# Optimization experiments

Hardware: AMD Instinct MI355X
Metric: run time of the kernel (lower is better)

Reference implementation:

```python
import jax, jax.numpy as jnp
import numpy as np
from jax import lax

K = 5          # dynamic kernel size
GROUPS = 8     # inter_channels // group_channels = 128 // 16
R = 2          # pixel shuffle upscale factor
SLOPE = 0.01   # LeakyReLU default negative_slope
EPS = 1e-5     # BatchNorm eps


def conv2d(x, w, b, pad=0):
    # x: [B,C,H,W], w: [O,I,kh,kw]
    y = lax.conv_general_dilated(x, w, (1, 1), [(pad, pad), (pad, pad)],
                                 dimension_numbers=('NCHW', 'OIHW', 'NCHW'))
    return y + b[None, :, None, None]


def pixel_shuffle(x, r):
    B, C, H, W = x.shape
    x = x.reshape(B, C // (r * r), r, r, H, W)
    x = x.transpose(0, 1, 4, 2, 5, 3)  # B, C', H, r, W, r
    return x.reshape(B, C // (r * r), H * r, W * r)


def involution(x, weight, k, groups, pad):
    # x: [B,C,H,W]; weight: [B,groups,k,k,H,W]
    # out[b, g*gc+c, h, w] = sum_ij weight[b,g,i,j,h,w] * x_pad[b, g*gc+c, h+i, w+j]
    B, C, H, W = x.shape
    gc = C // groups
    xp = jnp.pad(x, ((0, 0), (0, 0), (pad, pad), (pad, pad)))
    xg = xp.reshape(B, groups, gc, H + 2 * pad, W + 2 * pad)
    out = jnp.zeros((B, groups, gc, H, W), x.dtype)
    for i in range(k):
        for j in range(k):
            out = out + weight[:, :, None, i, j] * xg[:, :, :, i:i + H, j:j + W]
    return out.reshape(B, C, H, W)


def setup_inputs() -> dict:
    key = jax.random.key(0)
    ks = jax.random.split(key, 16)
    s = 0.05
    return {
        'high_level': jax.random.normal(ks[0], (8, 128, 64, 64), jnp.float32),
        'low_level': jax.random.normal(ks[1], (8, 224, 128, 128), jnp.float32),
        'emb': jax.random.normal(ks[2], (8, 256, 128, 128), jnp.float32),
        'reduce_w': jax.random.normal(ks[3], (128, 256, 1, 1), jnp.float32) * s,
        'reduce_b': jax.random.normal(ks[4], (128,), jnp.float32) * s,
        'conv1_w': jax.random.normal(ks[5], (32, 128, 1, 1), jnp.float32) * s,
        'conv1_b': jax.random.normal(ks[6], (32,), jnp.float32) * s,
        'conv2_w': jax.random.normal(ks[7], (200, 32, 3, 3), jnp.float32) * s,
        'conv2_b': jax.random.normal(ks[8], (200,), jnp.float32) * s,
        'embconv_w': jax.random.normal(ks[9], (32, 256, 1, 1), jnp.float32) * s,
        'embconv_b': jax.random.normal(ks[10], (32,), jnp.float32) * s,
        'out_w': jax.random.normal(ks[11], (64, 128, 1, 1), jnp.float32) * s,
        'out_b': jax.random.normal(ks[12], (64,), jnp.float32) * s,
        'bn_gamma': jnp.ones((64,), jnp.float32),
        'bn_beta': jnp.zeros((64,), jnp.float32),
        'bn_mean': jnp.zeros((64,), jnp.float32),
        'bn_var': jax.random.uniform(ks[13], (64,), jnp.float32, 0.5, 1.5),
    }


def reference(high_level, low_level, emb,
              reduce_w, reduce_b, conv1_w, conv1_b, conv2_w, conv2_b,
              embconv_w, embconv_b, out_w, out_b,
              bn_gamma, bn_beta, bn_mean, bn_var):
    cat = jnp.concatenate([pixel_shuffle(high_level, R), low_level], axis=1)
    cat = conv2d(cat, reduce_w, reduce_b)
    mix = jax.nn.leaky_relu(conv2d(cat, conv1_w, conv1_b)
                            + conv2d(emb, embconv_w, embconv_b), SLOPE)
    w = conv2d(mix, conv2_w, conv2_b, pad=1)  # [B, K*K*GROUPS, H, W]
    B, _, H, W = w.shape
    w = w.reshape(B, GROUPS, K, K, H, W)
    o = involution(cat, w, K, GROUPS, (K - 1) // 2)
    o = conv2d(o, out_w, out_b)
    o = (o - bn_mean[None, :, None, None]) * (bn_gamma[None, :, None, None]
        / jnp.sqrt(bn_var[None, :, None, None] + EPS)) + bn_beta[None, :, None, None]
    return jax.nn.leaky_relu(o, SLOPE)
```

## Files before the change

### kernel.cpp

```cpp
#include <hip/hip_runtime.h>

typedef unsigned short u16; typedef unsigned int u32; typedef unsigned long long u64;
typedef __attribute__((ext_vector_type(8))) short short8;
typedef __attribute__((ext_vector_type(16))) float f32x16;

#define HW 16384

#define RED_B  0
#define C1E_B  128
#define C2_B   160
#define OUT_B  416
#define BN_SC  480
#define BN_SH  544
#define FLAG_OFF   4096
#define RWB_OFF    8192
#define C1B_OFF    73728
#define EMBB_OFF   81920
#define OUTB_OFF   98304
#define C2PB_OFF   114688
#define CAT2_OFF   524288
#define MIX_OFF    34078720

__device__ __forceinline__ float bf2f(u16 x){ u32 u=((u32)x)<<16; float f; __builtin_memcpy(&f,&u,4); return f; }
__device__ __forceinline__ u16 f2bf(float f){ u32 u; __builtin_memcpy(&u,&f,4); return (u16)((u + 0x7fffu + ((u>>16)&1u))>>16); }
__device__ __forceinline__ u32 pk2(float a, float b){ return (u32)f2bf(a) | ((u32)f2bf(b)<<16); }
__device__ __forceinline__ float lrelu(float x){ return x>0.f ? x : 0.01f*x; }

template<int M> __device__ __forceinline__ u16 ldb(const void* p, size_t i){
    if (M==1) return ((const u16*)p)[i];
    return f2bf(((const float*)p)[i]);
}
template<int M> __device__ __forceinline__ float ldf(const void* p, size_t i){
    if (M==1) return bf2f(((const u16*)p)[i]);
    return ((const float*)p)[i];
}
__device__ __forceinline__ int swz(int p){ return ((p>>1) ^ (p>>3)) & 7; }

template<int M>
__device__ __forceinline__ void load8x8(const void* p, size_t base, size_t stride, u32 R[8][4]){
    if (M==1){
#pragma unroll
        for (int j=0;j<8;j++)
            __builtin_memcpy(&R[j][0], (const u16*)p + base + (size_t)j*stride, 16);
    } else {
        float raw[8][8];
#pragma unroll
        for (int j=0;j<8;j++)
            __builtin_memcpy(&raw[j][0], (const float*)p + base + (size_t)j*stride, 32);
#pragma unroll
        for (int j=0;j<8;j++)
#pragma unroll
        for (int m=0;m<4;m++) R[j][m] = pk2(raw[j][2*m], raw[j][2*m+1]);
    }
}

__global__ void detect_kernel(const void* __restrict__ emb, u32* __restrict__ flag){
    int tid = threadIdx.x;
    const u16* p = (const u16*)emb;
    int e = (p[tid*2] >> 7) & 0xFF;
    u64 m = __ballot(e >= 100 && e <= 140);
    if (tid == 0) *flag = (__popcll(m) >= 32) ? 1u : 0u;
}

template<int M>
__device__ __forceinline__ void prep_body(
    const void* rw, const void* rb, const void* c1w, const void* c1b,
    const void* c2w, const void* c2b, const void* ew, const void* eb,
    const void* ow, const void* ob, const void* gam, const void* bet,
    const void* mn, const void* vr, char* ws)
{
    float* wf = (float*)ws;
    int i = blockIdx.x*256 + threadIdx.x;
    if (i < 32768) {
        int o = i>>8, ic = i&255;
        int s = ic>>4, qq = (ic>>3)&1, e = ic&7;
        int dst = (((o>>5)*16 + s)*64 + qq*32 + (o&31))*8 + e;
        ((u16*)(ws+RWB_OFF))[dst] = ldb<M>(rw, i);
    }
    else if (i < 36864)  ((u16*)(ws+C1B_OFF))[i-32768] = ldb<M>(c1w, i-32768);
    else if (i < 45056)  ((u16*)(ws+EMBB_OFF))[i-36864] = ldb<M>(ew, i-36864);
    else if (i < 53248)  ((u16*)(ws+OUTB_OFF))[i-45056] = ldb<M>(ow, i-45056);
    else if (i < 126976) {
        int j = i-53248; int o = j/288, k = j - o*288;
        int tap = k>>5, ic = k&31;
        u16 v = 0;
        if (o < 200) v = ldb<M>(c2w, (size_t)o*288 + ic*9 + tap);
        ((u16*)(ws+C2PB_OFF))[j] = v;
    }
    else if (i < 127584) {
        int j = i-126976;
        if (j < 128) wf[RED_B+j] = ldf<M>(rb, j);
        else if (j < 160) wf[C1E_B+j-128] = ldf<M>(c1b, j-128) + ldf<M>(eb, j-128);
        else if (j < 416) { int o = j-160; wf[C2_B+o] = (o<200) ? ldf<M>(c2b,o) : 0.f; }
        else if (j < 480) wf[OUT_B+j-416] = ldf<M>(ob, j-416);
        else if (j < 544) { int c=j-480; wf[BN_SC+c] = ldf<M>(gam,c) * rsqrtf(ldf<M>(vr,c)+1e-5f); }
        else { int c=j-544; wf[BN_SH+c] = ldf<M>(bet,c) - ldf<M>(mn,c)*ldf<M>(gam,c)*rsqrtf(ldf<M>(vr,c)+1e-5f); }
    }
}

__global__ __launch_bounds__(256) void k_prep(
    const void* rw, const void* rb, const void* c1w, const void* c1b,
    const void* c2w, const void* c2b, const void* ew, const void* eb,
    const void* ow, const void* ob, const void* gam, const void* bet,
    const void* mn, const void* vr, char* ws, const u32* __restrict__ flag)
{
    if (*flag) prep_body<1>(rw,rb,c1w,c1b,c2w,c2b,ew,eb,ow,ob,gam,bet,mn,vr,ws);
    else       prep_body<0>(rw,rb,c1w,c1b,c2w,c2b,ew,eb,ow,ob,gam,bet,mn,vr,ws);
}

template<int M>
__device__ __forceinline__ void rm_body(
    const void* __restrict__ hi, const void* __restrict__ lo, const void* __restrict__ emb,
    const u16* __restrict__ rwB, const u16* __restrict__ c1B, const u16* __restrict__ embB,
    const float* __restrict__ wf, u16* __restrict__ cat2, u16* __restrict__ mixt,
    u16* At, u16* c2l)
{
    const int tid = threadIdx.x, wvi = tid>>6, lane = tid&63;
    const int col = lane&31, q = lane>>5;
    const int gpx = blockIdx.x*64;
    const int b = gpx>>14, p0 = gpx&16383;
    const int h = p0>>7, w0 = p0&127;
    const int co = tid>>3, po = tid&7;

    {
        u32 W[8][4];
        if (co < 28) {
            u32 R[8][4];
            load8x8<M>(lo, ((size_t)(b*224 + 8*co))*HW + p0 + 8*po, HW, R);
#pragma unroll
            for (int p=0;p<8;p++){
                const int u = p>>1, hf = p&1;
#pragma unroll
                for (int m=0;m<4;m++){
                    u32 A0 = R[2*m][u], A1 = R[2*m+1][u];
                    W[p][m] = hf ? ((A0>>16) | (A1 & 0xffff0000u))
                                 : ((A0 & 0xffffu) | (A1<<16));
                }
            }
            const int ch = co + 4;
#pragma unroll
            for (int p=0;p<8;p++){
                int pg = 8*po + p;
                __builtin_memcpy(At + pg*264 + ((ch ^ swz(pg))<<3), &W[p][0], 16);
            }
        } else {
            const int cc0 = (co-28)*8, h2 = (h&1)*2;
            u32 E[8][2], O[8][2];
            if (M==1){
#pragma unroll
                for (int j=0;j<8;j++){
                    int hc = (cc0+j)*4 + h2;
                    size_t src = ((size_t)(b*128 + hc))*4096 + (size_t)(h>>1)*64 + (w0>>1) + 4*po;
                    __builtin_memcpy(&E[j][0], (const u16*)hi + src, 8);
                    __builtin_memcpy(&O[j][0], (const u16*)hi + src + 4096, 8);
                }
            } else {
                float rE[8][4], rO[8][4];
#pragma unroll
                for (int j=0;j<8;j++){
                    int hc = (cc0+j)*4 + h2;
                    size_t src = ((size_t)(b*128 + hc))*4096 + (size_t)(h>>1)*64 + (w0>>1) + 4*po;
                    __builtin_memcpy(&rE[j][0], (const float*)hi + src, 16);
                    __builtin_memcpy(&rO[j][0], (const float*)hi + src + 4096, 16);
                }
#pragma unroll
                for (int j=0;j<8;j++){
                    E[j][0] = pk2(rE[j][0], rE[j][1]); E[j][1] = pk2(rE[j][2], rE[j][3]);
                    O[j][0] = pk2(rO[j][0], rO[j][1]); O[j][1] = pk2(rO[j][2], rO[j][3]);
                }
            }
#pragma unroll
            for (int p=0;p<8;p++){
                const int k = p>>1, u = k>>1, hf = k&1;
#pragma unroll
                for (int m=0;m<4;m++){
                    u32 A0, A1;
                    if (p&1){ A0 = O[2*m][u]; A1 = O[2*m+1][u]; }
                    else    { A0 = E[2*m][u]; A1 = E[2*m+1][u]; }
                    W[p][m] = hf ? ((A0>>16) | (A1 & 0xffff0000u))
                                 : ((A0 & 0xffffu) | (A1<<16));
                }
            }
            const int ch = co - 28;
#pragma unroll
            for (int p=0;p<8;p++){
                int pg = 8*po + p;
                __builtin_memcpy(At + pg*264 + ((ch ^ swz(pg))<<3), &W[p][0], 16);
            }
        }
    }
    __syncthreads();

    {
        const int rt = (wvi>>1)*32, nc0 = (wvi&1)*64;
        const int pp = rt + col, sw = swz(pp);
        const u16* arow = At + pp*264;
        const int ot0 = (wvi&1)*2;

        f32x16 acc0, acc1;
#pragma unroll
        for (int r=0;r<16;r++){ acc0[r]=0.f; acc1[r]=0.f; }

        short8 Bb[2][8];
#pragma unroll
        for (int nt=0;nt<2;nt++)
#pragma unroll
        for (int s=0;s<8;s++)
            __builtin_memcpy(&Bb[nt][s], rwB + (((size_t)((ot0+nt)*16 + s))*64 + lane)*8, 16);
#pragma unroll
        for (int s=0;s<8;s++){
            short8 a; __builtin_memcpy(&a, arow + (((2*s+q)^sw)<<3), 16);
            acc0 = __builtin_amdgcn_mfma_f32_32x32x16_bf16(a, Bb[0][s], acc0, 0,0,0);
            acc1 = __builtin_amdgcn_mfma_f32_32x32x16_bf16(a, Bb[1][s], acc1, 0,0,0);
        }
#pragma unroll
        for (int nt=0;nt<2;nt++)
#pragma unroll
        for (int s=0;s<8;s++)
            __builtin_memcpy(&Bb[nt][s], rwB + (((size_t)((ot0+nt)*16 + 8+s))*64 + lane)*8, 16);
#pragma unroll
        for (int s=8;s<16;s++){
            short8 a; __builtin_memcpy(&a, arow + (((2*s+q)^sw)<<3), 16);
            acc0 = __builtin_amdgcn_mfma_f32_32x32x16_bf16(a, Bb[0][s-8], acc0, 0,0,0);
            acc1 = __builtin_amdgcn_mfma_f32_32x32x16_bf16(a, Bb[1][s-8], acc1, 0,0,0);
        }

#pragma unroll
        for (int nt=0; nt<2; nt++){
            int oc = nc0 + nt*32 + col;
            float bias = wf[RED_B + oc];
#pragma unroll
            for (int r=0;r<16;r++){
                int row = (r&3) + 8*(r>>2) + 4*q;
                int px = rt + row;
                u16 bv = f2bf((nt ? acc1[r] : acc0[r]) + bias);
                cat2[((size_t)(gpx + px))*128 + oc] = bv;
                c2l[px*136 + (((oc>>3) ^ swz(px))<<3) + (oc&7)] = bv;
            }
        }
    }

    {
        u32 R[8][4];
        load8x8<M>(emb, ((size_t)(b*256 + 8*co))*HW + p0 + 8*po, HW, R);
        u32 W[8][4];
#pragma unroll
        for (int p=0;p<8;p++){
            const int u = p>>1, hf = p&1;
#pragma unroll
            for (int m=0;m<4;m++){
                u32 A0 = R[2*m][u], A1 = R[2*m+1][u];
                W[p][m] = hf ? ((A0>>16) | (A1 & 0xffff0000u))
                             : ((A0 & 0xffffu) | (A1<<16));
            }
        }
        __syncthreads();
#pragma unroll
        for (int p=0;p<8;p++){
            int pg = 8*po + p;
            __builtin_memcpy(At + pg*264 + ((co ^ swz(pg))<<3), &W[p][0], 16);
        }
    }
    __syncthreads();

    const int rt2 = wvi>>1, q2 = wvi&1;
    const int pp2 = rt2*32 + col, sw2 = swz(pp2);
    const u16* arow136 = c2l + pp2*136;
    const u16* arow264 = At + pp2*264;

    f32x16 macc;
#pragma unroll
    for (int r=0;r<16;r++) macc[r]=0.f;

    if (q2 == 0){
        short8 Bc[8];
#pragma unroll
        for (int s=0;s<8;s++)
            __builtin_memcpy(&Bc[s], c1B + (size_t)col*128 + s*16 + q*8, 16);
#pragma unroll
        for (int s=0;s<8;s++){
            short8 a; __builtin_memcpy(&a, arow136 + (((2*s+q)^sw2)<<3), 16);
            macc = __builtin_amdgcn_mfma_f32_32x32x16_bf16(a, Bc[s], macc, 0,0,0);
        }
        short8 Be[4];
#pragma unroll
        for (int s=0;s<4;s++)
            __builtin_memcpy(&Be[s], embB + (size_t)col*256 + s*16 + q*8, 16);
#pragma unroll
        for (int s=0;s<4;s++){
            short8 a; __builtin_memcpy(&a, arow264 + (((2*s+q)^sw2)<<3), 16);
            macc = __builtin_amdgcn_mfma_f32_32x32x16_bf16(a, Be[s], macc, 0,0,0);
        }
    } else {
        short8 Be[12];
#pragma unroll
        for (int s=0;s<12;s++)
            __builtin_memcpy(&Be[s], embB + (size_t)col*256 + (4+s)*16 + q*8, 16);
#pragma unroll
        for (int s=0;s<12;s++){
            int ks = 4 + s;
            short8 a; __builtin_memcpy(&a, arow264 + (((2*ks+q)^sw2)<<3), 16);
            macc = __builtin_amdgcn_mfma_f32_32x32x16_bf16(a, Be[s], macc, 0,0,0);
        }
    }
    __syncthreads();

    float* exch = (float*)At;
    if (q2 == 1){
#pragma unroll
        for (int r=0;r<16;r++){
            int row = (r&3) + 8*(r>>2) + 4*q;
            exch[rt2*1024 + row*32 + col] = macc[r];
        }
    }
    __syncthreads();
    if (q2 == 0){
        float bias = wf[C1E_B + col];
#pragma unroll
        for (int r=0;r<16;r++){
            int row = (r&3) + 8*(r>>2) + 4*q;
            float v = macc[r] + exch[rt2*1024 + row*32 + col] + bias;
            mixt[((size_t)(gpx + rt2*32 + row))*32 + col] = f2bf(lrelu(v));
        }
    }
}

__global__ __launch_bounds__(256,2) void k_rm(
    const void* __restrict__ hi, const void* __restrict__ lo, const void* __restrict__ emb,
    const u16* __restrict__ rwB, const u16* __restrict__ c1B, const u16* __restrict__ embB,
    const float* __restrict__ wf, u16* __restrict__ cat2, u16* __restrict__ mixt,
    const u32* __restrict__ flag)
{
    __shared__ u16 At[64*264];
    __shared__ u16 c2l[64*136];
    if (*flag) rm_body<1>(hi, lo, emb, rwB, c1B, embB, wf, cat2, mixt, At, c2l);
    else       rm_body<0>(hi, lo, emb, rwB, c1B, embB, wf, cat2, mixt, At, c2l);
}

template<int M>
__device__ __forceinline__ void inv_body(
    const u16* __restrict__ cat2, const u16* __restrict__ mixt,
    const u16* __restrict__ c2B, const u16* __restrict__ outB,
    const float* __restrict__ wf, void* __restrict__ out,
    u16* halo_m, u16* wgt_l, u16* halo_c, u16* og)
{
    const int tid = threadIdx.x, wvi = tid>>6, lane = tid&63;
    const int col = lane&31, q = lane>>5;
    const int b = blockIdx.y, ty = blockIdx.x>>3, tx = blockIdx.x&7;
    const int py = tid>>4, px = tid&15;

    f32x16 acc[2][2];
#pragma unroll
    for (int i=0;i<2;i++)
#pragma unroll
    for (int j=0;j<2;j++)
#pragma unroll
    for (int r=0;r<16;r++) acc[i][j][r] = 0.f;

#pragma unroll
    for (int i=0;i<6;i++){
        int idx = tid + i*256;
        if (idx < 1296){
            int point = idx>>2, cq = idx&3;
            int y = ty*16 + point/18 - 1, x = tx*16 + point%18 - 1;
            short8 v;
            if (y>=0 && y<128 && x>=0 && x<128)
                __builtin_memcpy(&v, mixt + ((size_t)(b*HW + y*128 + x))*32 + cq*8, 16);
            else { short z=0; v = (short8){z,z,z,z,z,z,z,z}; }
            *(short8*)(halo_m + point*40 + cq*8) = v;
        }
    }
    __syncthreads();

#pragma unroll 1
    for (int g=0; g<8; g++){
        __syncthreads();

        const int o = g*25 + col;
        short8 Bf[18];
#pragma unroll
        for (int s=0;s<18;s++)
            __builtin_memcpy(&Bf[s], c2B + (size_t)o*288 + s*16 + q*8, 16);

#pragma unroll
        for (int i=0;i<4;i++){
            int idx = tid + i*256;
            if (idx < 800){
                int point = idx>>1, cq = idx&1;
                int y = ty*16 + point/20 - 2, x = tx*16 + point%20 - 2;
                short8 v;
                if (y>=0 && y<128 && x>=0 && x<128)
                    __builtin_memcpy(&v, cat2 + ((size_t)(b*HW + y*128 + x))*128 + g*16 + cq*8, 16);
                else { short z=0; v = (short8){z,z,z,z,z,z,z,z}; }
                *(short8*)(halo_c + point*16 + cq*8) = v;
            }
        }

        f32x16 c0, c1;
#pragma unroll
        for (int r=0;r<16;r++){ c0[r]=0.f; c1[r]=0.f; }
        const int p0 = wvi*64 + col, p1 = p0 + 32;
        const int pya = p0>>4, pxa = p0&15, pyb = p1>>4, pxb = p1&15;
#pragma unroll
        for (int s=0;s<18;s++){
            int tap = s>>1, ih = s&1;
            int dy = tap/3, dx = tap%3;
            short8 a0, a1;
            __builtin_memcpy(&a0, halo_m + ((pya+dy)*18 + pxa+dx)*40 + ih*16 + q*8, 16);
            __builtin_memcpy(&a1, halo_m + ((pyb+dy)*18 + pxb+dx)*40 + ih*16 + q*8, 16);
            c0 = __builtin_amdgcn_mfma_f32_32x32x16_bf16(a0, Bf[s], c0, 0,0,0);
            c1 = __builtin_amdgcn_mfma_f32_32x32x16_bf16(a1, Bf[s], c1, 0,0,0);
        }
        {
            float bias = wf[C2_B + o];
#pragma unroll
            for (int rt2=0; rt2<2; rt2++){
                int mb = wvi*64 + rt2*32;
#pragma unroll
                for (int r=0;r<16;r+=2){
                    int row0 = (r&3) + 8*(r>>2) + 4*q;
                    float v0 = (rt2 ? c1[r]   : c0[r])   + bias;
                    float v1 = (rt2 ? c1[r+1] : c0[r+1]) + bias;
                    u32 pkv = (u32)f2bf(v0) | ((u32)f2bf(v1)<<16);
                    *(u32*)(wgt_l + (size_t)col*264 + mb + row0) = pkv;
                }
            }
        }
        __syncthreads();

        float wvv[25];
#pragma unroll
        for (int t=0;t<25;t++) wvv[t] = bf2f(wgt_l[t*264 + tid]);

        float a16[16];
#pragma unroll
        for (int cc=0;cc<16;cc++) a16[cc]=0.f;
#pragma unroll
        for (int t=0;t<25;t++){
            int dy = t/5, dx = t%5;
            u32 vv[8];
            __builtin_memcpy(vv, halo_c + ((py+dy)*20 + px+dx)*16, 32);
            float wt = wvv[t];
#pragma unroll
            for (int r=0;r<8;r++){
                u32 u = vv[r];
                u32 ulo = u<<16, uhi = u & 0xffff0000u;
                float x0, x1;
                __builtin_memcpy(&x0,&ulo,4); __builtin_memcpy(&x1,&uhi,4);
                a16[2*r]   += wt*x0;
                a16[2*r+1] += wt*x1;
            }
        }
        u32 pk[8];
#pragma unroll
        for (int r=0;r<8;r++) pk[r] = (u32)f2bf(a16[2*r]) | ((u32)f2bf(a16[2*r+1])<<16);
        __builtin_memcpy(og + tid*16, pk, 32);
        __syncthreads();

        short8 bo0, bo1;
        __builtin_memcpy(&bo0, outB + (size_t)(col)*128      + g*16 + q*8, 16);
        __builtin_memcpy(&bo1, outB + (size_t)(32+col)*128   + g*16 + q*8, 16);
#pragma unroll
        for (int rt2=0; rt2<2; rt2++){
            int prow = (wvi*2 + rt2)*32 + col;
            short8 a; __builtin_memcpy(&a, og + prow*16 + q*8, 16);
            acc[rt2][0] = __builtin_amdgcn_mfma_f32_32x32x16_bf16(a, bo0, acc[rt2][0], 0,0,0);
            acc[rt2][1] = __builtin_amdgcn_mfma_f32_32x32x16_bf16(a, bo1, acc[rt2][1], 0,0,0);
        }
    }
#pragma unroll
    for (int rt2=0; rt2<2; rt2++)
#pragma unroll
    for (int nt=0; nt<2; nt++){
        int oc = nt*32 + col;
        float bias = wf[OUT_B+oc], sc = wf[BN_SC+oc], sh = wf[BN_SH+oc];
#pragma unroll
        for (int r=0;r<16;r++){
            int row = (r&3) + 8*(r>>2) + 4*q;
            int p = (wvi*2 + rt2)*32 + row;
            int yy = ty*16 + (p>>4), xx = tx*16 + (p&15);
            float v = lrelu((acc[rt2][nt][r] + bias)*sc + sh);
            size_t oidx = ((size_t)(b*64 + oc))*HW + yy*128 + xx;
            if (M==1) ((u16*)out)[oidx] = f2bf(v);
            else ((float*)out)[oidx] = v;
        }
    }
}

__global__ __launch_bounds__(256,2) void k_inv(
    const u16* __restrict__ cat2, const u16* __restrict__ mixt,
    const u16* __restrict__ c2B, const u16* __restrict__ outB,
    const float* __restrict__ wf, void* __restrict__ out, const u32* __restrict__ flag)
{
    __shared__ u16 halo_m[324*40];
    __shared__ u16 wgt_l[32*264];
    __shared__ u16 halo_c[400*16];
    __shared__ u16 og[256*16];
    if (*flag) inv_body<1>(cat2, mixt, c2B, outB, wf, out, halo_m, wgt_l, halo_c, og);
    else       inv_body<0>(cat2, mixt, c2B, outB, wf, out, halo_m, wgt_l, halo_c, og);
}

extern "C" void kernel_launch(void* const* d_in, const int* in_sizes, int n_in,
                              void* d_out, int out_size, void* d_ws, size_t ws_size,
                              hipStream_t stream) {
    const void* hi  = d_in[0];
    const void* lo  = d_in[1];
    const void* emb = d_in[2];
    char* ws = (char*)d_ws;
    float* wf = (float*)ws;
    u32* flag = (u32*)(ws + FLAG_OFF);
    u16* cat2 = (u16*)(ws + CAT2_OFF);
    u16* mixt = (u16*)(ws + MIX_OFF);

    detect_kernel<<<1, 64, 0, stream>>>(emb, flag);

    k_prep<<<499,256,0,stream>>>(d_in[3],d_in[4],d_in[5],d_in[6],d_in[7],d_in[8],
        d_in[9],d_in[10],d_in[11],d_in[12],d_in[13],d_in[14],d_in[15],d_in[16], ws, flag);

    k_rm<<<2048,256,0,stream>>>(hi, lo, emb, (const u16*)(ws+RWB_OFF),
                                (const u16*)(ws+C1B_OFF), (const u16*)(ws+EMBB_OFF),
                                wf, cat2, mixt, flag);

    k_inv<<<dim3(64,8),256,0,stream>>>(cat2, mixt, (const u16*)(ws+C2PB_OFF),
                                       (const u16*)(ws+OUTB_OFF), wf, d_out, flag);
}
```

Before: 396.2 us.

## Fold conv1 into reduce weights and split reduce/mix GEMMs across 512 threads

Precomputes a combined conv1·reduce weight (and folded bias) in the prep kernel, so the mix branch multiplies the raw concatenated input directly instead of waiting for the reduced cat tensor. This removes the dependency and the extra LDS staging buffer. k_rm now runs 512 threads, with half preloading emb while the other half builds the cat tile, and the K dimension split across four waves with a cross-wave reduction. The k_rm kernel is templated on the input-format flag and launched twice, with early exit in the non-matching variant. The folded weight is rounded to bf16, which changes numerics slightly.

```diff
diff --git a/kernel.cpp b/kernel.cpp
--- a/kernel.cpp
+++ b/kernel.cpp
@@ -18,6 +18,7 @@
 #define EMBB_OFF   81920
 #define OUTB_OFF   98304
 #define C2PB_OFF   114688
+#define WEFF_OFF   262144
 #define CAT2_OFF   524288
 #define MIX_OFF    34078720
 
@@ -35,24 +36,6 @@
     return ((const float*)p)[i];
 }
 __device__ __forceinline__ int swz(int p){ return ((p>>1) ^ (p>>3)) & 7; }
-
-template<int M>
-__device__ __forceinline__ void load8x8(const void* p, size_t base, size_t stride, u32 R[8][4]){
-    if (M==1){
-#pragma unroll
-        for (int j=0;j<8;j++)
-            __builtin_memcpy(&R[j][0], (const u16*)p + base + (size_t)j*stride, 16);
-    } else {
-        float raw[8][8];
-#pragma unroll
-        for (int j=0;j<8;j++)
-            __builtin_memcpy(&raw[j][0], (const float*)p + base + (size_t)j*stride, 32);
-#pragma unroll
-        for (int j=0;j<8;j++)
-#pragma unroll
-        for (int m=0;m<4;m++) R[j][m] = pk2(raw[j][2*m], raw[j][2*m+1]);
-    }
-}
 
 __global__ void detect_kernel(const void* __restrict__ emb, u32* __restrict__ flag){
     int tid = threadIdx.x;
@@ -90,11 +73,26 @@
     else if (i < 127584) {
         int j = i-126976;
         if (j < 128) wf[RED_B+j] = ldf<M>(rb, j);
-        else if (j < 160) wf[C1E_B+j-128] = ldf<M>(c1b, j-128) + ldf<M>(eb, j-128);
+        else if (j < 160) {
+            int o = j-128;
+            float s = ldf<M>(c1b,o) + ldf<M>(eb,o);
+#pragma unroll 8
+            for (int ic=0; ic<128; ic++)
+                s += ldf<M>(c1w, (size_t)o*128+ic) * ldf<M>(rb, ic);
+            wf[C1E_B+o] = s;
+        }
         else if (j < 416) { int o = j-160; wf[C2_B+o] = (o<200) ? ldf<M>(c2b,o) : 0.f; }
         else if (j < 480) wf[OUT_B+j-416] = ldf<M>(ob, j-416);
         else if (j < 544) { int c=j-480; wf[BN_SC+c] = ldf<M>(gam,c) * rsqrtf(ldf<M>(vr,c)+1e-5f); }
         else { int c=j-544; wf[BN_SH+c] = ldf<M>(bet,c) - ldf<M>(mn,c)*ldf<M>(gam,c)*rsqrtf(ldf<M>(vr,c)+1e-5f); }
+    }
+    else if (i < 135776) {
+        int j = i - 127584; int oc = j>>8, k2 = j&255;
+        float s = 0.f;
+#pragma unroll 8
+        for (int ic=0; ic<128; ic++)
+            s += ldf<M>(c1w, (size_t)oc*128+ic) * ldf<M>(rw, (size_t)ic*256+k2);
+        ((u16*)(ws+WEFF_OFF))[oc*256+k2] = f2bf(s);
     }
 }
 
@@ -111,22 +109,68 @@
 template<int M>
 __device__ __forceinline__ void rm_body(
     const void* __restrict__ hi, const void* __restrict__ lo, const void* __restrict__ emb,
-    const u16* __restrict__ rwB, const u16* __restrict__ c1B, const u16* __restrict__ embB,
+    const u16* __restrict__ rwB, const u16* __restrict__ weffB, const u16* __restrict__ embB,
     const float* __restrict__ wf, u16* __restrict__ cat2, u16* __restrict__ mixt,
-    u16* At, u16* c2l)
+    u16* At)
 {
     const int tid = threadIdx.x, wvi = tid>>6, lane = tid&63;
     const int col = lane&31, q = lane>>5;
     const int gpx = blockIdx.x*64;
     const int b = gpx>>14, p0 = gpx&16383;
     const int h = p0>>7, w0 = p0&127;
-    const int co = tid>>3, po = tid&7;
-
-    {
+
+    const int sthr = tid & 255;
+    const int co = sthr>>3, po = sthr&7;
+    const bool is_emb = tid >= 256;
+
+    u32 Wreg[8][4];
+
+    if (is_emb) {
+        u32 R[8][4];
+        size_t base = ((size_t)(b*256 + 8*co))*HW + p0 + 8*po;
+        if (M==1){
+#pragma unroll
+            for (int j=0;j<8;j++)
+                __builtin_memcpy(&R[j][0], (const u16*)emb + base + (size_t)j*HW, 16);
+        } else {
+            float raw[8][8];
+#pragma unroll
+            for (int j=0;j<8;j++)
+                __builtin_memcpy(&raw[j][0], (const float*)emb + base + (size_t)j*HW, 32);
+#pragma unroll
+            for (int j=0;j<8;j++)
+#pragma unroll
+            for (int m=0;m<4;m++) R[j][m] = pk2(raw[j][2*m], raw[j][2*m+1]);
+        }
+#pragma unroll
+        for (int p=0;p<8;p++){
+            const int u = p>>1, hf = p&1;
+#pragma unroll
+            for (int m=0;m<4;m++){
+                u32 A0 = R[2*m][u], A1 = R[2*m+1][u];
+                Wreg[p][m] = hf ? ((A0>>16) | (A1 & 0xffff0000u))
+                                : ((A0 & 0xffffu) | (A1<<16));
+            }
+        }
+    } else {
         u32 W[8][4];
         if (co < 28) {
             u32 R[8][4];
-            load8x8<M>(lo, ((size_t)(b*224 + 8*co))*HW + p0 + 8*po, HW, R);
+            size_t base = ((size_t)(b*224 + 8*co))*HW + p0 + 8*po;
+            if (M==1){
+#pragma unroll
+                for (int j=0;j<8;j++)
+                    __builtin_memcpy(&R[j][0], (const u16*)lo + base + (size_t)j*HW, 16);
+            } else {
+                float raw[8][8];
+#pragma unroll
+                for (int j=0;j<8;j++)
+                    __builtin_memcpy(&raw[j][0], (const float*)lo + base + (size_t)j*HW, 32);
+#pragma unroll
+                for (int j=0;j<8;j++)
+#pragma unroll
+                for (int m=0;m<4;m++) R[j][m] = pk2(raw[j][2*m], raw[j][2*m+1]);
+            }
 #pragma unroll
             for (int p=0;p<8;p++){
                 const int u = p>>1, hf = p&1;
@@ -191,150 +235,100 @@
     }
     __syncthreads();
 
+    const int pt = wvi>>2, ks = wvi&3;
+    const int pp = pt*32 + col, sw = swz(pp);
+    const u16* arow = At + pp*264;
+
+    f32x16 racc, macc;
+#pragma unroll
+    for (int r=0;r<16;r++){ racc[r]=0.f; macc[r]=0.f; }
+
+    short8 Wf[4];
+#pragma unroll
+    for (int t4=0;t4<4;t4++)
+        __builtin_memcpy(&Wf[t4], weffB + (size_t)col*256 + (4*ks+t4)*16 + q*8, 16);
+
+#pragma unroll
+    for (int bt=0; bt<4; bt++){
+        short8 Bb[4];
+#pragma unroll
+        for (int si=0;si<4;si++)
+            __builtin_memcpy(&Bb[si], rwB + (((size_t)(ks*16 + bt*4 + si))*64 + lane)*8, 16);
+#pragma unroll
+        for (int si=0;si<4;si++){
+            int s = bt*4 + si;
+            short8 a; __builtin_memcpy(&a, arow + (((2*s+q)^sw)<<3), 16);
+            racc = __builtin_amdgcn_mfma_f32_32x32x16_bf16(a, Bb[si], racc, 0,0,0);
+            int d = s - 4*ks;
+            if (d>=0 && d<4)
+                macc = __builtin_amdgcn_mfma_f32_32x32x16_bf16(a, Wf[d], macc, 0,0,0);
+        }
+    }
     {
-        const int rt = (wvi>>1)*32, nc0 = (wvi&1)*64;
-        const int pp = rt + col, sw = swz(pp);
-        const u16* arow = At + pp*264;
-        const int ot0 = (wvi&1)*2;
-
-        f32x16 acc0, acc1;
-#pragma unroll
-        for (int r=0;r<16;r++){ acc0[r]=0.f; acc1[r]=0.f; }
-
-        short8 Bb[2][8];
-#pragma unroll
-        for (int nt=0;nt<2;nt++)
-#pragma unroll
-        for (int s=0;s<8;s++)
-            __builtin_memcpy(&Bb[nt][s], rwB + (((size_t)((ot0+nt)*16 + s))*64 + lane)*8, 16);
-#pragma unroll
-        for (int s=0;s<8;s++){
-            short8 a; __builtin_memcpy(&a, arow + (((2*s+q)^sw)<<3), 16);
-            acc0 = __builtin_amdgcn_mfma_f32_32x32x16_bf16(a, Bb[0][s], acc0, 0,0,0);
-            acc1 = __builtin_amdgcn_mfma_f32_32x32x16_bf16(a, Bb[1][s], acc1, 0,0,0);
-        }
-#pragma unroll
-        for (int nt=0;nt<2;nt++)
-#pragma unroll
-        for (int s=0;s<8;s++)
-            __builtin_memcpy(&Bb[nt][s], rwB + (((size_t)((ot0+nt)*16 + 8+s))*64 + lane)*8, 16);
-#pragma unroll
-        for (int s=8;s<16;s++){
-            short8 a; __builtin_memcpy(&a, arow + (((2*s+q)^sw)<<3), 16);
-            acc0 = __builtin_amdgcn_mfma_f32_32x32x16_bf16(a, Bb[0][s-8], acc0, 0,0,0);
-            acc1 = __builtin_amdgcn_mfma_f32_32x32x16_bf16(a, Bb[1][s-8], acc1, 0,0,0);
-        }
-
-#pragma unroll
-        for (int nt=0; nt<2; nt++){
-            int oc = nc0 + nt*32 + col;
-            float bias = wf[RED_B + oc];
-#pragma unroll
-            for (int r=0;r<16;r++){
-                int row = (r&3) + 8*(r>>2) + 4*q;
-                int px = rt + row;
-                u16 bv = f2bf((nt ? acc1[r] : acc0[r]) + bias);
-                cat2[((size_t)(gpx + px))*128 + oc] = bv;
-                c2l[px*136 + (((oc>>3) ^ swz(px))<<3) + (oc&7)] = bv;
-            }
-        }
-    }
-
-    {
-        u32 R[8][4];
-        load8x8<M>(emb, ((size_t)(b*256 + 8*co))*HW + p0 + 8*po, HW, R);
-        u32 W[8][4];
-#pragma unroll
-        for (int p=0;p<8;p++){
-            const int u = p>>1, hf = p&1;
-#pragma unroll
-            for (int m=0;m<4;m++){
-                u32 A0 = R[2*m][u], A1 = R[2*m+1][u];
-                W[p][m] = hf ? ((A0>>16) | (A1 & 0xffff0000u))
-                             : ((A0 & 0xffffu) | (A1<<16));
-            }
-        }
-        __syncthreads();
+        int oc = ks*32 + col;
+        float bias = wf[RED_B + oc];
+#pragma unroll
+        for (int r=0;r<16;r++){
+            int row = (r&3) + 8*(r>>2) + 4*q;
+            cat2[((size_t)(gpx + pt*32 + row))*128 + oc] = f2bf(racc[r] + bias);
+        }
+    }
+    __syncthreads();
+
+    if (is_emb){
 #pragma unroll
         for (int p=0;p<8;p++){
             int pg = 8*po + p;
-            __builtin_memcpy(At + pg*264 + ((co ^ swz(pg))<<3), &W[p][0], 16);
+            __builtin_memcpy(At + pg*264 + ((co ^ swz(pg))<<3), &Wreg[p][0], 16);
         }
     }
     __syncthreads();
 
-    const int rt2 = wvi>>1, q2 = wvi&1;
-    const int pp2 = rt2*32 + col, sw2 = swz(pp2);
-    const u16* arow136 = c2l + pp2*136;
-    const u16* arow264 = At + pp2*264;
-
-    f32x16 macc;
-#pragma unroll
-    for (int r=0;r<16;r++) macc[r]=0.f;
-
-    if (q2 == 0){
-        short8 Bc[8];
-#pragma unroll
-        for (int s=0;s<8;s++)
-            __builtin_memcpy(&Bc[s], c1B + (size_t)col*128 + s*16 + q*8, 16);
-#pragma unroll
-        for (int s=0;s<8;s++){
-            short8 a; __builtin_memcpy(&a, arow136 + (((2*s+q)^sw2)<<3), 16);
-            macc = __builtin_amdgcn_mfma_f32_32x32x16_bf16(a, Bc[s], macc, 0,0,0);
-        }
+    {
         short8 Be[4];
 #pragma unroll
-        for (int s=0;s<4;s++)
-            __builtin_memcpy(&Be[s], embB + (size_t)col*256 + s*16 + q*8, 16);
-#pragma unroll
-        for (int s=0;s<4;s++){
-            short8 a; __builtin_memcpy(&a, arow264 + (((2*s+q)^sw2)<<3), 16);
-            macc = __builtin_amdgcn_mfma_f32_32x32x16_bf16(a, Be[s], macc, 0,0,0);
-        }
-    } else {
-        short8 Be[12];
-#pragma unroll
-        for (int s=0;s<12;s++)
-            __builtin_memcpy(&Be[s], embB + (size_t)col*256 + (4+s)*16 + q*8, 16);
-#pragma unroll
-        for (int s=0;s<12;s++){
-            int ks = 4 + s;
-            short8 a; __builtin_memcpy(&a, arow264 + (((2*ks+q)^sw2)<<3), 16);
-            macc = __builtin_amdgcn_mfma_f32_32x32x16_bf16(a, Be[s], macc, 0,0,0);
+        for (int t4=0;t4<4;t4++)
+            __builtin_memcpy(&Be[t4], embB + (size_t)col*256 + (4*ks+t4)*16 + q*8, 16);
+#pragma unroll
+        for (int t4=0;t4<4;t4++){
+            int t = 4*ks + t4;
+            short8 a; __builtin_memcpy(&a, arow + (((2*t+q)^sw)<<3), 16);
+            macc = __builtin_amdgcn_mfma_f32_32x32x16_bf16(a, Be[t4], macc, 0,0,0);
         }
     }
     __syncthreads();
 
     float* exch = (float*)At;
-    if (q2 == 1){
+    if (ks != 0){
 #pragma unroll
         for (int r=0;r<16;r++){
             int row = (r&3) + 8*(r>>2) + 4*q;
-            exch[rt2*1024 + row*32 + col] = macc[r];
+            exch[pt*3072 + (ks-1)*1024 + row*32 + col] = macc[r];
         }
     }
     __syncthreads();
-    if (q2 == 0){
+    if (ks == 0){
         float bias = wf[C1E_B + col];
 #pragma unroll
         for (int r=0;r<16;r++){
             int row = (r&3) + 8*(r>>2) + 4*q;
-            float v = macc[r] + exch[rt2*1024 + row*32 + col] + bias;
-            mixt[((size_t)(gpx + rt2*32 + row))*32 + col] = f2bf(lrelu(v));
-        }
-    }
-}
-
-__global__ __launch_bounds__(256,2) void k_rm(
+            int base = pt*3072 + row*32 + col;
+            float v = macc[r] + exch[base] + exch[base+1024] + exch[base+2048] + bias;
+            mixt[((size_t)(gpx + pt*32 + row))*32 + col] = f2bf(lrelu(v));
+        }
+    }
+}
+
+template<int M>
+__global__ __launch_bounds__(512,4) void k_rm(
     const void* __restrict__ hi, const void* __restrict__ lo, const void* __restrict__ emb,
-    const u16* __restrict__ rwB, const u16* __restrict__ c1B, const u16* __restrict__ embB,
+    const u16* __restrict__ rwB, const u16* __restrict__ weffB, const u16* __restrict__ embB,
     const float* __restrict__ wf, u16* __restrict__ cat2, u16* __restrict__ mixt,
     const u32* __restrict__ flag)
 {
+    if (*flag != (u32)M) return;
     __shared__ u16 At[64*264];
-    __shared__ u16 c2l[64*136];
-    if (*flag) rm_body<1>(hi, lo, emb, rwB, c1B, embB, wf, cat2, mixt, At, c2l);
-    else       rm_body<0>(hi, lo, emb, rwB, c1B, embB, wf, cat2, mixt, At, c2l);
+    rm_body<M>(hi, lo, emb, rwB, weffB, embB, wf, cat2, mixt, At);
 }
 
 template<int M>
@@ -514,12 +508,15 @@
 
     detect_kernel<<<1, 64, 0, stream>>>(emb, flag);
 
-    k_prep<<<499,256,0,stream>>>(d_in[3],d_in[4],d_in[5],d_in[6],d_in[7],d_in[8],
+    k_prep<<<531,256,0,stream>>>(d_in[3],d_in[4],d_in[5],d_in[6],d_in[7],d_in[8],
         d_in[9],d_in[10],d_in[11],d_in[12],d_in[13],d_in[14],d_in[15],d_in[16], ws, flag);
 
-    k_rm<<<2048,256,0,stream>>>(hi, lo, emb, (const u16*)(ws+RWB_OFF),
-                                (const u16*)(ws+C1B_OFF), (const u16*)(ws+EMBB_OFF),
-                                wf, cat2, mixt, flag);
+    k_rm<1><<<2048,512,0,stream>>>(hi, lo, emb, (const u16*)(ws+RWB_OFF),
+                                   (const u16*)(ws+WEFF_OFF), (const u16*)(ws+EMBB_OFF),
+                                   wf, cat2, mixt, flag);
+    k_rm<0><<<2048,512,0,stream>>>(hi, lo, emb, (const u16*)(ws+RWB_OFF),
+                                   (const u16*)(ws+WEFF_OFF), (const u16*)(ws+EMBB_OFF),
+                                   wf, cat2, mixt, flag);
 
     k_inv<<<dim3(64,8),256,0,stream>>>(cat2, mixt, (const u16*)(ws+C2PB_OFF),
                                        (const u16*)(ws+OUTB_OFF), wf, d_out, flag);
```

Measured after the change: 430.9 us. 1.09x slower.
